# Kernel tuning notes

Measured on AMD Instinct MI355X. Metric: run time of the kernel, lower is better.

Reference implementation:

```python
import jax, jax.numpy as jnp
import numpy as np

B, C, H, W = 8, 256, 128, 128
S = C // 4          # squeezed channels (squeeze_factor=4)
HEADS = 8

def _conv(x, w, pad, groups=1):
    # NCHW conv, stride 1
    return jax.lax.conv_general_dilated(
        x, w, (1, 1), [(pad, pad), (pad, pad)],
        feature_group_count=groups,
        dimension_numbers=('NCHW', 'OIHW', 'NCHW'))

def _cln(x, w, b):
    # WithBias LayerNorm over channel dim (to_3d -> LN over c -> to_4d)
    mu = jnp.mean(x, axis=1, keepdims=True)
    var = jnp.mean((x - mu) ** 2, axis=1, keepdims=True)
    return (x - mu) * jax.lax.rsqrt(var + 1e-5) * w[None, :, None, None] + b[None, :, None, None]

def setup_inputs() -> dict:
    key = jax.random.key(0)
    ks = jax.random.split(key, 14)
    r = lambda i, shape, s=0.05: jax.random.normal(ks[i], shape, jnp.float32) * s
    return dict(
        x=r(0, (B, C, H, W), 1.0),
        y=r(1, (B, C, H, W), 1.0),
        w_cq=r(2, (S, C, 3, 3)),          # compress_q
        w_ckv=r(3, (S, C, 3, 3)),         # compress_kv
        ln_q_w=jnp.ones(S), ln_q_b=jnp.zeros(S),
        ln_kv_w=jnp.ones(S), ln_kv_b=jnp.zeros(S),
        w_kv=r(4, (2 * S, S, 1, 1)),      # kv 1x1
        w_kvdw=r(5, (2 * S, 1, 3, 3)),    # kv depthwise 3x3
        w_q=r(6, (S, S, 3, 3)),           # q 3x3
        temperature=jnp.ones((HEADS, 1, 1)),
        w_po=r(7, (S, S, 1, 1)),          # project_out 1x1
        w_expand=r(8, (C, S, 3, 3)),      # expand 3x3
        ln_out_w=jnp.ones(C), ln_out_b=jnp.zeros(C),
        w_ffn1=r(9, (C, 2 * C, 1, 1)),    # ffn conv1x1 (dim_q+dim_kv -> dim_out)
        w_ffn_dw=r(10, (C, 1, 3, 3)),     # ffn depthwise 3x3
        w_ffn2=r(11, (C, C, 1, 1)),       # ffn conv1x1
    )

def reference(x, y, w_cq, w_ckv, ln_q_w, ln_q_b, ln_kv_w, ln_kv_b,
              w_kv, w_kvdw, w_q, temperature, w_po, w_expand,
              ln_out_w, ln_out_b, w_ffn1, w_ffn_dw, w_ffn2):
    # channel compress + LayerNorm
    xq = _cln(_conv(x, w_cq, 1), ln_q_w, ln_q_b)      # [B,S,H,W]
    ykv = _cln(_conv(y, w_ckv, 1), ln_kv_w, ln_kv_b)  # [B,S,H,W]
    b, c, h, w = xq.shape
    # cross channel attention
    kv = _conv(_conv(ykv, w_kv, 0), w_kvdw, 1, groups=2 * c)
    k, v = jnp.split(kv, 2, axis=1)
    q = _conv(xq, w_q, 1)
    sh = lambda t: t.reshape(b, HEADS, c // HEADS, h * w)  # b head c (hw)
    q, k, v = sh(q), sh(k), sh(v)
    q = q / jnp.maximum(jnp.linalg.norm(q, axis=-1, keepdims=True), 1e-12)
    k = k / jnp.maximum(jnp.linalg.norm(k, axis=-1, keepdims=True), 1e-12)
    attn = jax.nn.softmax(
        jnp.einsum('bhcn,bhdn->bhcd', q, k) * temperature[None], axis=-1)
    o = jnp.einsum('bhcd,bhdn->bhcn', attn, v).reshape(b, c, h, w)
    o = _conv(o, w_po, 0)
    # expand back to full channels, norm, conv FFN
    vexp = _conv(o, w_expand, 1)                      # [B,C,H,W]
    vn = _cln(vexp, ln_out_w, ln_out_b)
    cat = jnp.concatenate([x, vn], axis=1)            # [B,2C,H,W]
    f = _conv(cat, w_ffn1, 0)
    f = jax.nn.gelu(_conv(f, w_ffn_dw, 1, groups=f.shape[1]), approximate=False)
    return _conv(f, w_ffn2, 0)
```

## Files before the change

kernel.cpp:

```cpp
#include <hip/hip_runtime.h>
#include <hip/hip_bf16.h>
#include <math.h>

#define B_ 8
#define C_ 256
#define S_ 64
#define H_ 128
#define W_ 128
#define HW_ (H_*W_)
#define P_ (B_*HW_)

typedef __attribute__((ext_vector_type(8))) short short8;
typedef __attribute__((ext_vector_type(4))) float f32x4;

__device__ __forceinline__ unsigned short f2b(float f){
    __hip_bfloat16 h = __float2bfloat16(f);
    return *reinterpret_cast<unsigned short*>(&h);
}
__device__ __forceinline__ void up8(uint4 u, float* f){
    unsigned v0=u.x,v1=u.y,v2=u.z,v3=u.w;
    f[0]=__uint_as_float(v0<<16); f[1]=__uint_as_float(v0&0xffff0000u);
    f[2]=__uint_as_float(v1<<16); f[3]=__uint_as_float(v1&0xffff0000u);
    f[4]=__uint_as_float(v2<<16); f[5]=__uint_as_float(v2&0xffff0000u);
    f[6]=__uint_as_float(v3<<16); f[7]=__uint_as_float(v3&0xffff0000u);
}
__device__ __forceinline__ uint4 pk8(const float* f){
    uint4 u;
    u.x = (unsigned)f2b(f[0]) | ((unsigned)f2b(f[1])<<16);
    u.y = (unsigned)f2b(f[2]) | ((unsigned)f2b(f[3])<<16);
    u.z = (unsigned)f2b(f[4]) | ((unsigned)f2b(f[5])<<16);
    u.w = (unsigned)f2b(f[6]) | ((unsigned)f2b(f[7])<<16);
    return u;
}
__device__ __forceinline__ void gl2lds(const unsigned short* g, unsigned short* l){
    __builtin_amdgcn_global_load_lds((const __attribute__((address_space(1))) void*)g,
                                     (__attribute__((address_space(3))) void*)l, 16, 0, 0);
}


__global__ __launch_bounds__(256) void pack_k(const float* __restrict__ inA,
                                              const float* __restrict__ inB,
                                              unsigned short* __restrict__ outA,
                                              unsigned short* __restrict__ outB)
{
    __shared__ unsigned short tl[64][72];
    const int t = threadIdx.x;
    const int p0 = blockIdx.x*64, c0 = blockIdx.y*64;
    const int sel = blockIdx.z >> 3, b = blockIdx.z & 7;
    const float* in = sel ? inB : inA;
    unsigned short* out = sel ? outB : outA;
    const float* ib = in + ((size_t)b*C_ + c0)*HW_ + p0;
    for (int i = t; i < 1024; i += 256){
        int ci = i >> 4, px = (i & 15)*4;
        float4 v = *(const float4*)(ib + (size_t)ci*HW_ + px);
        tl[px+0][ci]=f2b(v.x); tl[px+1][ci]=f2b(v.y); tl[px+2][ci]=f2b(v.z); tl[px+3][ci]=f2b(v.w);
    }
    __syncthreads();
    for (int i = t; i < 512; i += 256){
        int px = i >> 3, c8 = (i & 7)*8;
        int cc = c0 + c8;
        unsigned short* dst = out + ((size_t)b*8 + (cc>>5))*(size_t)HW_*32
                                  + (size_t)(p0+px)*32 + (cc&31);
        *(uint4*)dst = *(uint4*)&tl[px][c8];
    }
}

__device__ __forceinline__ void packw(const float* __restrict__ src, unsigned short* __restrict__ dst,
                                      int e, int CO, int CI, int KS2)
{
    int KB = CI/32;
    int tap = e / (CO*CI);
    int rem = e % (CO*CI);
    int coT = rem / (CI*16);
    int rem2 = rem % (CI*16);
    int kb = rem2 >> 9;
    int l  = (rem2 >> 3) & 63;
    int ee = rem2 & 7;
    int co = coT*16 + (l & 15);
    int ci = kb*32 + (l >> 4)*8 + ee;
    float v = (KS2==9) ? src[(size_t)(co*CI+ci)*9 + tap] : src[(size_t)co*CI + ci];
    dst[e] = f2b(v);
}

__global__ __launch_bounds__(256) void prep_k(const float* __restrict__ cq, const float* __restrict__ ckv,
                                              const float* __restrict__ q,  const float* __restrict__ kv,
                                              const float* __restrict__ f1, const float* __restrict__ f2,
                                              const float* __restrict__ dwk, const float* __restrict__ dwf,
                                              unsigned short* o_cq, unsigned short* o_ckv, unsigned short* o_q,
                                              unsigned short* o_kv, unsigned short* o_f1, unsigned short* o_f2,
                                              unsigned short* o_dwk, unsigned short* o_dwf)
{
    int i = blockIdx.x*256 + threadIdx.x;
    if      (i < 147456) packw(cq,  o_cq,  i,          64, 256, 9);
    else if (i < 294912) packw(ckv, o_ckv, i-147456,   64, 256, 9);
    else if (i < 331776) packw(q,   o_q,   i-294912,   64,  64, 9);
    else if (i < 339968) packw(kv,  o_kv,  i-331776,  128,  64, 1);
    else if (i < 471040) packw(f1,  o_f1,  i-339968,  256, 512, 1);
    else if (i < 536576) packw(f2,  o_f2,  i-471040,  256, 256, 1);
    else if (i < 537728) { int e=i-536576; o_dwk[e] = f2b(dwk[(e&127)*9 + (e>>7)]); }
    else if (i < 540032) { int e=i-537728; o_dwf[e] = f2b(dwf[(e&255)*9 + (e>>8)]); }
    else if (i < 540040) { o_dwf[i-537728] = 0; }
}

template<int C0,int C1,int COUT,int KS,int OUTM,int LNF>
__global__ __launch_bounds__(256,4) void mconv_k(
    const unsigned short* __restrict__ in0, int s0,
    const unsigned short* __restrict__ in1, int s1,
    const unsigned short* __restrict__ wp, long wpbs,
    void* __restrict__ outp, int so,
    const unsigned short* __restrict__ in0B,
    const unsigned short* __restrict__ wpB2,
    void* __restrict__ outB,
    const unsigned short* __restrict__ zbuf,
    const float* __restrict__ lnw0, const float* __restrict__ lnb0,
    const float* __restrict__ lnw1, const float* __restrict__ lnb1,
    int ny, int nz)
{
    constexpr int CINT = C0+C1;
    constexpr int KB  = CINT/32;
    constexpr int MT  = 4;
    constexpr int NT  = 2;
    constexpr int PXS = (KS==3)?66:128;
    constexpr int ASZ = (KS==3)? 4*66*32 : 8192;
    constexpr int EP  = (OUTM==1) ? 64*132*2 : 128*64;
    constexpr int SSZ = (2*ASZ > EP) ? 2*ASZ : EP;
    __shared__ alignas(16) unsigned short sbuf[SSZ];

    const int t = threadIdx.x;
    const int nper = (128*ny*nz) >> 3;
    int lin = (blockIdx.x & 7)*nper + (blockIdx.x >> 3);
    const int gy_ = lin % ny;
    int rem = lin / ny;
    const int gx_ = rem & 127;
    const int gz_ = rem >> 7;
    const int sel = gz_ >> 3;
    const int b   = gz_ & 7;
    const int cob = gy_*64;

    const unsigned short* pin0 = sel ? in0B : in0;
    const unsigned short* wpb  = (sel ? wpB2 : wp) + (size_t)b*wpbs;

    int y0=0,x0=0; size_t p0=0;
    if (KS==3){ y0=(gx_>>1)*2; x0=(gx_&1)*64; }
    else p0 = (size_t)gx_*128;

    const int l = t&63, w = t>>6;
    const int wy = w>>1, wx = w&1;
    const int lrow = l&15, lk = l>>4;

    const size_t b0base = (size_t)b*HW_*s0;
    const size_t b1base = (size_t)b*HW_*s1;

    auto issueA3 = [&](int kb, int bsel){
        const int cg = kb*32;
        unsigned short* dst = sbuf + bsel*ASZ;
        #pragma unroll
        for (int j=0;j<5;++j){
            int i = t + j*256;
            if (j<4 || i<1056){
                int slot = i&3, pr = i>>2;
                int px = pr%66, row = pr/66;
                int g = slot ^ (px&3) ^ ((px>>2)&3);
                int c = cg + g*8;
                int gy = y0+row-1, gx = x0+px-1;
                bool ok = ((unsigned)gy<(unsigned)H_) & ((unsigned)gx<(unsigned)W_);
                size_t p = (size_t)gy*W_+gx;
                const unsigned short* base = (c<C0)
                    ? pin0 + b0base + ((size_t)(c>>5)*HW_ + p)*32 + (c&31)
                    : in1  + b1base + ((size_t)((c-C0)>>5)*HW_ + p)*32 + ((c-C0)&31);
                gl2lds(ok ? base : zbuf, dst + (size_t)i*8);
            }
        }
    };
    auto issueA1 = [&](int s, int bsel){
        unsigned short* dst = sbuf + bsel*ASZ;
        #pragma unroll
        for (int h=0;h<2;++h){
            const int cg = (s*2+h)*32;
            #pragma unroll
            for (int j=0;j<2;++j){
                int i = t + j*256;
                int slot = i&3, px = i>>2;
                int g = slot ^ (px&3) ^ ((px>>2)&3);
                int c = cg + g*8;
                size_t p = p0+px;
                const unsigned short* sp = (c<C0)
                    ? pin0 + b0base + ((size_t)(c>>5)*HW_ + p)*32 + (c&31)
                    : in1  + b1base + ((size_t)((c-C0)>>5)*HW_ + p)*32 + ((c-C0)&31);
                gl2lds(sp, dst + (size_t)(h*4096 + i*8));
            }
        }
    };
    auto loadB = [&](short8* dst, int kb, int tap){
        #pragma unroll
        for (int n=0;n<NT;++n){
            int fi = (tap*(COUT/16) + (cob>>4) + wx*NT + n)*KB + kb;
            dst[n] = *(const short8*)(wpb + (size_t)fi*512 + l*8);
        }
    };

    f32x4 acc[MT][NT] = {};

    if (KS==3){
        short8 bfs[3][NT];
        issueA3(0,0);
        loadB(bfs[0],0,0); loadB(bfs[1],0,1); loadB(bfs[2],0,2);
        for (int kb=0; kb<KB; ++kb){
            __syncthreads();
            if (kb+1<KB) issueA3(kb+1,(kb+1)&1);
            unsigned short* cur = sbuf + (kb&1)*ASZ;
            #pragma unroll
            for (int tap=0;tap<9;++tap){
                const int ky=tap/3, kx=tap%3;
                short8 af[MT];
                #pragma unroll
                for (int m=0;m<MT;++m){
                    int pl = wy*64 + m*16 + lrow;
                    int r = (pl>>6)+ky, xx = (pl&63)+kx;
                    af[m] = *(const short8*)&cur[((r*PXS+xx)*4 + (lk^(xx&3)^((xx>>2)&3)))*8];
                }
                #pragma unroll
                for (int m=0;m<MT;++m)
                    #pragma unroll
                    for (int n=0;n<NT;++n)
                        acc[m][n] = __builtin_amdgcn_mfma_f32_16x16x32_bf16(af[m],bfs[tap%3][n],acc[m][n],0,0,0);
                if (tap+3 < 9)      loadB(bfs[tap%3], kb, tap+3);
                else if (kb+1<KB)   loadB(bfs[tap%3], kb+1, tap-6);
            }
        }
    } else {
        constexpr int KBS = (KB>=2) ? KB/2 : 1;
        short8 bfs[2][NT];
        issueA1(0,0);
        loadB(bfs[0],0,0); loadB(bfs[1],1,0);
        for (int s=0; s<KBS; ++s){
            __syncthreads();
            if (s+1<KBS) issueA1(s+1,(s+1)&1);
            unsigned short* cur = sbuf + (s&1)*ASZ;
            #pragma unroll
            for (int j=0;j<2;++j){
                short8 af[MT];
                #pragma unroll
                for (int m=0;m<MT;++m){
                    int pl = wy*64 + m*16 + lrow;
                    af[m] = *(const short8*)&cur[j*4096 + (pl*4 + (lk^(pl&3)^((pl>>2)&3)))*8];
                }
                #pragma unroll
                for (int m=0;m<MT;++m)
                    #pragma unroll
                    for (int n=0;n<NT;++n)
                        acc[m][n] = __builtin_amdgcn_mfma_f32_16x16x32_bf16(af[m],bfs[j][n],acc[m][n],0,0,0);
                if (s*2+j+2 < KB) loadB(bfs[j], s*2+j+2, 0);
            }
        }
    }
    __syncthreads();

    if (OUTM==1){
        float* sf = (float*)sbuf;
        #pragma unroll
        for (int m=0;m<MT;++m)
            #pragma unroll
            for (int n=0;n<NT;++n){
                int co_l = wx*32 + n*16 + lrow;
                int pl0  = wy*64 + m*16 + lk*4;
                *(f32x4*)&sf[co_l*132 + pl0] = acc[m][n];
            }
        __syncthreads();
        float* out = (float*)(sel ? outB : outp);
        for (int i=t; i<2048; i+=256){
            int co = i>>5, pxg = i&31;
            f32x4 v = *(const f32x4*)&sf[co*132 + pxg*4];
            *(f32x4*)(out + ((size_t)(b*COUT + cob + co))*HW_ + p0 + pxg*4) = v;
        }
    } else if (LNF){
        #pragma unroll
        for (int m=0;m<MT;++m)
            #pragma unroll
            for (int n=0;n<NT;++n){
                int co = wx*32 + n*16 + lrow;
                int grp = co>>3, cr = co&7;
                #pragma unroll
                for (int r=0;r<4;++r){
                    int pl = wy*64 + m*16 + lk*4 + r;
                    sbuf[pl*64 + ((grp^(pl&7))<<3) + cr] = f2b(acc[m][n][r]);
                }
            }
        __syncthreads();
        if (t < 128){
            int pl = t;
            uint4 raw[8];
            float s = 0.f, ss = 0.f;
            #pragma unroll
            for (int j=0;j<8;++j){
                raw[j] = *(const uint4*)&sbuf[pl*64 + ((j^(pl&7))<<3)];
                float f[8]; up8(raw[j], f);
                #pragma unroll
                for (int k=0;k<8;++k){ s += f[k]; ss += f[k]*f[k]; }
            }
            float mu = s*(1.f/64.f);
            float rs = rsqrtf(ss*(1.f/64.f) - mu*mu + 1e-5f);
            const float* lw = sel ? lnw1 : lnw0;
            const float* lb = sel ? lnb1 : lnb0;
            unsigned short* out = (unsigned short*)(sel ? outB : outp);
            size_t p = (size_t)(y0+(pl>>6))*W_ + x0 + (pl&63);
            #pragma unroll
            for (int j=0;j<8;++j){
                float f[8], o[8];
                up8(raw[j], f);
                #pragma unroll
                for (int k=0;k<8;++k) o[k] = (f[k]-mu)*rs*lw[j*8+k] + lb[j*8+k];
                int cc = j*8;
                unsigned short* dst = out + ((size_t)b*2 + (cc>>5))*(size_t)HW_*32 + p*32 + (cc&31);
                *(uint4*)dst = pk8(o);
            }
        }
    } else {
        unsigned short* out = (unsigned short*)(sel ? outB : outp);
        #pragma unroll
        for (int m=0;m<MT;++m)
            #pragma unroll
            for (int n=0;n<NT;++n){
                int co = wx*32 + n*16 + lrow;
                #pragma unroll
                for (int r=0;r<4;++r){
                    int pl = wy*64 + m*16 + lk*4 + r;
                    sbuf[pl*64 + co] = f2b(acc[m][n][r]);
                }
            }
        __syncthreads();
        for (int i=t; i<1024; i+=256){
            int pl = i>>3, c8 = (i&7)*8;
            size_t p = (KS==3) ? ((size_t)(y0+(pl>>6))*W_ + (size_t)(x0+(pl&63))) : (p0+pl);
            int cc = cob + c8;
            unsigned short* dst = out + (size_t)b*HW_*so + ((size_t)(cc>>5)*HW_ + p)*32 + (cc&31);
            *(uint4*)dst = *(uint4*)&sbuf[pl*64 + c8];
        }
    }
}

template<int C>
__global__ __launch_bounds__(256) void cln_k(unsigned short* __restrict__ io,
                                             const float* __restrict__ wg,
                                             const float* __restrict__ bi)
{
    constexpr int L = C/8;
    size_t idx = (size_t)blockIdx.x*256 + threadIdx.x;
    int sub = (int)(idx % L);
    size_t pix = idx / L;
    int b = (int)(pix >> 14);
    size_t p = pix & (HW_-1);
    unsigned short* rp = io + ((size_t)b*(C/32) + (sub>>2))*(size_t)HW_*32 + p*32 + (sub&3)*8;
    uint4 raw = *(const uint4*)rp;
    float f[8]; up8(raw, f);
    float s = 0.f, ss = 0.f;
    #pragma unroll
    for (int j=0;j<8;++j){ s += f[j]; ss += f[j]*f[j]; }
    #pragma unroll
    for (int m=1;m<L;m<<=1){ s += __shfl_xor(s,m); ss += __shfl_xor(ss,m); }
    float mu = s*(1.f/C);
    float rs = rsqrtf(ss*(1.f/C) - mu*mu + 1e-5f);
    float4 w0 = *(const float4*)(wg+sub*8), w1 = *(const float4*)(wg+sub*8+4);
    float4 b0 = *(const float4*)(bi+sub*8), b1 = *(const float4*)(bi+sub*8+4);
    float o[8];
    o[0]=(f[0]-mu)*rs*w0.x+b0.x; o[1]=(f[1]-mu)*rs*w0.y+b0.y;
    o[2]=(f[2]-mu)*rs*w0.z+b0.z; o[3]=(f[3]-mu)*rs*w0.w+b0.w;
    o[4]=(f[4]-mu)*rs*w1.x+b1.x; o[5]=(f[5]-mu)*rs*w1.y+b1.y;
    o[6]=(f[6]-mu)*rs*w1.z+b1.z; o[7]=(f[7]-mu)*rs*w1.w+b1.w;
    *(uint4*)rp = pk8(o);
}

template<int CH, bool GELU>
__global__ __launch_bounds__(256) void dw_k(const unsigned short* __restrict__ in,
                                            const unsigned short* __restrict__ wp,
                                            unsigned short* __restrict__ out)
{
    size_t idx = (size_t)blockIdx.x*256 + threadIdx.x;
    int c8 = (int)(idx % (CH/8));
    size_t pix = idx / (CH/8);
    int p = (int)(pix % HW_);
    int b = (int)(pix / HW_);
    int yy = p >> 7, xx = p & 127;
    const unsigned short* ib = in + ((size_t)b*(CH/32) + (c8>>2))*(size_t)HW_*32 + (c8&3)*8;
    float wf[9][8];
    #pragma unroll
    for (int tap=0; tap<9; ++tap){
        uint4 r = *(const uint4*)(wp + tap*CH + c8*8);
        up8(r, wf[tap]);
    }
    float a[8] = {0,0,0,0,0,0,0,0};
    #pragma unroll
    for (int ky=0; ky<3; ++ky){
        int gy = yy+ky-1;
        if ((unsigned)gy >= (unsigned)H_) continue;
        #pragma unroll
        for (int kx=0; kx<3; ++kx){
            int gx = xx+kx-1;
            if ((unsigned)gx >= (unsigned)W_) continue;
            uint4 r = *(const uint4*)(ib + (size_t)(gy*W_+gx)*32);
            float f[8]; up8(r, f);
            #pragma unroll
            for (int j=0;j<8;++j) a[j] += f[j]*wf[ky*3+kx][j];
        }
    }
    if (GELU){
        #pragma unroll
        for (int j=0;j<8;++j) a[j] = 0.5f*a[j]*(1.f + erff(a[j]*0.70710678118654752f));
    }
    unsigned short* ob = out + ((size_t)b*(CH/32) + (c8>>2))*(size_t)HW_*32 + (size_t)p*32 + (c8&3)*8;
    *(uint4*)ob = pk8(a);
}

__global__ __launch_bounds__(256) void attn_k(const unsigned short* __restrict__ qc,
                                              const unsigned short* __restrict__ kvd,
                                              const float* __restrict__ temp,
                                              float* __restrict__ probs)
{
    int b = blockIdx.x >> 3, h = blockIdx.x & 7;
    int t = threadIdx.x;
    const unsigned short* qb = qc  + ((size_t)b*2 + (h>>2))*(size_t)HW_*32 + (h&3)*8;
    const unsigned short* kb = kvd + ((size_t)b*4 + (h>>2))*(size_t)HW_*32 + (h&3)*8;
    float qs[8] = {}, ks[8] = {}, dt[8][8] = {{}};
    for (int p = t; p < HW_; p += 256){
        float qv[8], kv[8];
        up8(*(const uint4*)(qb + (size_t)p*32), qv);
        up8(*(const uint4*)(kb + (size_t)p*32), kv);
        #pragma unroll
        for (int i=0;i<8;++i){ qs[i]+=qv[i]*qv[i]; ks[i]+=kv[i]*kv[i]; }
        #pragma unroll
        for (int i=0;i<8;++i)
            #pragma unroll
            for (int j=0;j<8;++j) dt[i][j] += qv[i]*kv[j];
    }
    __shared__ float red[4][80];
    __shared__ float fin[80];
    int lane = t & 63, wv = t >> 6;
    #pragma unroll
    for (int i=0;i<8;++i){ float v=qs[i]; for (int m=1;m<64;m<<=1) v += __shfl_xor(v,m); if(!lane) red[wv][i]=v; }
    #pragma unroll
    for (int i=0;i<8;++i){ float v=ks[i]; for (int m=1;m<64;m<<=1) v += __shfl_xor(v,m); if(!lane) red[wv][8+i]=v; }
    #pragma unroll
    for (int i=0;i<8;++i)
        #pragma unroll
        for (int j=0;j<8;++j){ float v=dt[i][j]; for (int m=1;m<64;m<<=1) v += __shfl_xor(v,m); if(!lane) red[wv][16+i*8+j]=v; }
    __syncthreads();
    if (t < 80) fin[t] = red[0][t]+red[1][t]+red[2][t]+red[3][t];
    __syncthreads();
    if (t < 8){
        int i = t;
        float qn = fmaxf(sqrtf(fin[i]), 1e-12f);
        float tm = temp[h];
        float lg[8]; float mx = -1e30f;
        #pragma unroll
        for (int j=0;j<8;++j){
            float kn = fmaxf(sqrtf(fin[8+j]), 1e-12f);
            lg[j] = fin[16+i*8+j]/(qn*kn)*tm;
            mx = fmaxf(mx, lg[j]);
        }
        float se = 0.f;
        #pragma unroll
        for (int j=0;j<8;++j){ lg[j]=expf(lg[j]-mx); se+=lg[j]; }
        float inv = 1.f/se;
        #pragma unroll
        for (int j=0;j<8;++j) probs[(((size_t)b*8+h)*8+i)*8+j] = lg[j]*inv;
    }
}

__global__ __launch_bounds__(256) void mb_k(const float* __restrict__ probs,
                                            const float* __restrict__ wpo,
                                            float* __restrict__ Mb)
{
    int b = blockIdx.x;
    for (int o = threadIdx.x; o < 4096; o += 256){
        int co = o >> 6, d = o & 63, h = d >> 3, j = d & 7;
        float s = 0.f;
        #pragma unroll
        for (int i2=0;i2<8;++i2)
            s += wpo[co*64 + h*8 + i2] * probs[(((size_t)b*8+h)*8+i2)*8 + j];
        Mb[(size_t)b*4096 + o] = s;
    }
}

__global__ __launch_bounds__(256) void weff_k(const float* __restrict__ Mb,
                                              const float* __restrict__ wex,
                                              unsigned short* __restrict__ weff)
{
    int b = blockIdx.x / 576;
    int i = (blockIdx.x % 576)*256 + threadIdx.x;
    int tap = i / 16384;
    int rem = i % 16384;
    int coT = rem / 1024;
    int rem2 = rem % 1024;
    int kb = rem2 >> 9;
    int l  = (rem2 >> 3) & 63;
    int ee = rem2 & 7;
    int eo = coT*16 + (l & 15);
    int d  = kb*32 + (l >> 4)*8 + ee;
    const float* mb = Mb + (size_t)b*4096;
    float s = 0.f;
    #pragma unroll 8
    for (int c=0;c<64;++c)
        s += wex[(size_t)(eo*64+c)*9 + tap] * mb[c*64 + d];
    weff[(size_t)b*147456 + i] = f2b(s);
}

extern "C" void kernel_launch(void* const* d_in, const int* in_sizes, int n_in,
                              void* d_out, int out_size, void* d_ws, size_t ws_size,
                              hipStream_t stream) {
    (void)in_sizes; (void)n_in; (void)out_size; (void)ws_size;
    const float* x        = (const float*)d_in[0];
    const float* y        = (const float*)d_in[1];
    const float* w_cq     = (const float*)d_in[2];
    const float* w_ckv    = (const float*)d_in[3];
    const float* ln_q_w   = (const float*)d_in[4];
    const float* ln_q_b   = (const float*)d_in[5];
    const float* ln_kv_w  = (const float*)d_in[6];
    const float* ln_kv_b  = (const float*)d_in[7];
    const float* w_kv     = (const float*)d_in[8];
    const float* w_kvdw   = (const float*)d_in[9];
    const float* w_q      = (const float*)d_in[10];
    const float* temperature = (const float*)d_in[11];
    const float* w_po     = (const float*)d_in[12];
    const float* w_expand = (const float*)d_in[13];
    const float* ln_out_w = (const float*)d_in[14];
    const float* ln_out_b = (const float*)d_in[15];
    const float* w_ffn1   = (const float*)d_in[16];
    const float* w_ffn_dw = (const float*)d_in[17];
    const float* w_ffn2   = (const float*)d_in[18];
    float* outp = (float*)d_out;

    const size_t MB = 1u<<20;
    char* ws8 = (char*)d_ws;
    unsigned short* ykv  = (unsigned short*)(ws8 + 0);
    unsigned short* xq   = (unsigned short*)(ws8 + 16*MB);
    unsigned short* kv1  = (unsigned short*)(ws8 + 32*MB);
    unsigned short* qc   = (unsigned short*)(ws8 + 64*MB);
    unsigned short* kvd  = (unsigned short*)(ws8 + 80*MB);
    unsigned short* vexp = (unsigned short*)(ws8 + 0);
    unsigned short* f2b_ = (unsigned short*)(ws8 + 0);
    float* probs = (float*)(ws8 + 112*MB);
    float* Mb    = (float*)(ws8 + 113*MB);
    unsigned short* weff = (unsigned short*)(ws8 + 114*MB);
    unsigned short* wpB  = (unsigned short*)(ws8 + 117*MB);
    unsigned short* wp_cq  = wpB;
    unsigned short* wp_ckv = wpB + 147456;
    unsigned short* wp_q   = wpB + 294912;
    unsigned short* wp_kv  = wpB + 331776;
    unsigned short* wp_f1  = wpB + 339968;
    unsigned short* wp_f2  = wpB + 471040;
    unsigned short* wp_dwk = wpB + 536576;
    unsigned short* wp_dwf = wpB + 537728;
    unsigned short* zbuf   = wpB + 540032;
    unsigned short* xb = (unsigned short*)d_out;
    unsigned short* yb = (unsigned short*)d_out + 32*MB;
    unsigned short* f1 = yb;

    const unsigned short* NUL = (const unsigned short*)nullptr;

    prep_k<<<2111, 256, 0, stream>>>(w_cq, w_ckv, w_q, w_kv, w_ffn1, w_ffn2, w_kvdw, w_ffn_dw,
                                     wp_cq, wp_ckv, wp_q, wp_kv, wp_f1, wp_f2, wp_dwk, wp_dwf);
    pack_k<<<dim3(256,4,16), 256, 0, stream>>>(y, x, yb, xb);
    mconv_k<256,0,64,3,0,1><<<128*1*16, 256, 0, stream>>>(yb,256, NUL,0, wp_ckv,0, ykv,64,
        xb, wp_cq, xq, zbuf, ln_kv_w, ln_kv_b, ln_q_w, ln_q_b, 1, 16);
    mconv_k<64,0,128,1,0,0><<<128*2*8, 256, 0, stream>>>(ykv,64, NUL,0, wp_kv,0, kv1,128,
        ykv, wp_kv, kv1, zbuf, NULL,NULL,NULL,NULL, 2, 8);
    mconv_k<64,0,64,3,0,0><<<128*1*8, 256, 0, stream>>>(xq,64, NUL,0, wp_q,0, qc,64,
        xq, wp_q, qc, zbuf, NULL,NULL,NULL,NULL, 1, 8);
    dw_k<128,false><<<8192, 256, 0, stream>>>(kv1, wp_dwk, kvd);
    attn_k<<<64, 256, 0, stream>>>(qc, kvd, temperature, probs);
    mb_k<<<8, 256, 0, stream>>>(probs, w_po, Mb);
    weff_k<<<4608, 256, 0, stream>>>(Mb, w_expand, weff);
    mconv_k<64,0,256,3,0,0><<<128*4*8, 256, 0, stream>>>(kvd + (size_t)HW_*64,128, NUL,0, weff,147456, vexp,256,
        kvd + (size_t)HW_*64, weff, vexp, zbuf, NULL,NULL,NULL,NULL, 4, 8);
    cln_k<256><<<16384, 256, 0, stream>>>(vexp, ln_out_w, ln_out_b);
    mconv_k<256,256,256,1,0,0><<<128*4*8, 256, 0, stream>>>(xb,256, vexp,256, wp_f1,0, f1,256,
        xb, wp_f1, f1, zbuf, NULL,NULL,NULL,NULL, 4, 8);
    dw_k<256,true><<<16384, 256, 0, stream>>>(f1, wp_dwf, f2b_);
    mconv_k<256,0,256,1,1,0><<<128*4*8, 256, 0, stream>>>(f2b_,256, NUL,0, wp_f2,0, outp,0,
        f2b_, wp_f2, outp, zbuf, NULL,NULL,NULL,NULL, 4, 8);
}
```

Baseline: 519.3 us.

## Double pixel tile per block in mconv_k and widen warp N-tiles

```diff
diff --git a/kernel.cpp b/kernel.cpp
--- a/kernel.cpp
+++ b/kernel.cpp
@@ -103,7 +103,7 @@
 }
 
 template<int C0,int C1,int COUT,int KS,int OUTM,int LNF>
-__global__ __launch_bounds__(256,4) void mconv_k(
+__global__ __launch_bounds__(256,3) void mconv_k(
     const unsigned short* __restrict__ in0, int s0,
     const unsigned short* __restrict__ in1, int s1,
     const unsigned short* __restrict__ wp, long wpbs,
@@ -119,20 +119,21 @@
     constexpr int CINT = C0+C1;
     constexpr int KB  = CINT/32;
     constexpr int MT  = 4;
-    constexpr int NT  = 2;
-    constexpr int PXS = (KS==3)?66:128;
-    constexpr int ASZ = (KS==3)? 4*66*32 : 8192;
-    constexpr int EP  = (OUTM==1) ? 64*132*2 : 128*64;
+    constexpr int NT  = 4;
+    constexpr int PXS = (KS==3)?66:256;
+    constexpr int NTR = (KS==3)? 6*66*4 : 256*4;
+    constexpr int ASZ = NTR*8;
+    constexpr int EP  = (OUTM==1) ? 64*132*2 : 256*64;
     constexpr int SSZ = (2*ASZ > EP) ? 2*ASZ : EP;
     __shared__ alignas(16) unsigned short sbuf[SSZ];
 
     const int t = threadIdx.x;
-    const int nper = (128*ny*nz) >> 3;
+    const int nper = (64*ny*nz) >> 3;
     int lin = (blockIdx.x & 7)*nper + (blockIdx.x >> 3);
     const int gy_ = lin % ny;
     int rem = lin / ny;
-    const int gx_ = rem & 127;
-    const int gz_ = rem >> 7;
+    const int gx_ = rem & 63;
+    const int gz_ = rem >> 6;
     const int sel = gz_ >> 3;
     const int b   = gz_ & 7;
     const int cob = gy_*64;
@@ -141,11 +142,10 @@
     const unsigned short* wpb  = (sel ? wpB2 : wp) + (size_t)b*wpbs;
 
     int y0=0,x0=0; size_t p0=0;
-    if (KS==3){ y0=(gx_>>1)*2; x0=(gx_&1)*64; }
-    else p0 = (size_t)gx_*128;
-
-    const int l = t&63, w = t>>6;
-    const int wy = w>>1, wx = w&1;
+    if (KS==3){ y0=(gx_>>1)*4; x0=(gx_&1)*64; }
+    else p0 = (size_t)gx_*256;
+
+    const int l = t&63, wv = t>>6;
     const int lrow = l&15, lk = l>>4;
 
     const size_t b0base = (size_t)b*HW_*s0;
@@ -155,9 +155,9 @@
         const int cg = kb*32;
         unsigned short* dst = sbuf + bsel*ASZ;
         #pragma unroll
-        for (int j=0;j<5;++j){
+        for (int j=0;j<7;++j){
             int i = t + j*256;
-            if (j<4 || i<1056){
+            if (j<6 || i<1584){
                 int slot = i&3, pr = i>>2;
                 int px = pr%66, row = pr/66;
                 int g = slot ^ (px&3) ^ ((px>>2)&3);
@@ -172,29 +172,26 @@
             }
         }
     };
-    auto issueA1 = [&](int s, int bsel){
+    auto issueA1 = [&](int kb, int bsel){
+        const int cg = kb*32;
         unsigned short* dst = sbuf + bsel*ASZ;
         #pragma unroll
-        for (int h=0;h<2;++h){
-            const int cg = (s*2+h)*32;
-            #pragma unroll
-            for (int j=0;j<2;++j){
-                int i = t + j*256;
-                int slot = i&3, px = i>>2;
-                int g = slot ^ (px&3) ^ ((px>>2)&3);
-                int c = cg + g*8;
-                size_t p = p0+px;
-                const unsigned short* sp = (c<C0)
-                    ? pin0 + b0base + ((size_t)(c>>5)*HW_ + p)*32 + (c&31)
-                    : in1  + b1base + ((size_t)((c-C0)>>5)*HW_ + p)*32 + ((c-C0)&31);
-                gl2lds(sp, dst + (size_t)(h*4096 + i*8));
-            }
+        for (int j=0;j<4;++j){
+            int i = t + j*256;
+            int slot = i&3, px = i>>2;
+            int g = slot ^ (px&3) ^ ((px>>2)&3);
+            int c = cg + g*8;
+            size_t p = p0+px;
+            const unsigned short* sp = (c<C0)
+                ? pin0 + b0base + ((size_t)(c>>5)*HW_ + p)*32 + (c&31)
+                : in1  + b1base + ((size_t)((c-C0)>>5)*HW_ + p)*32 + ((c-C0)&31);
+            gl2lds(sp, dst + (size_t)i*8);
         }
     };
     auto loadB = [&](short8* dst, int kb, int tap){
         #pragma unroll
         for (int n=0;n<NT;++n){
-            int fi = (tap*(COUT/16) + (cob>>4) + wx*NT + n)*KB + kb;
+            int fi = (tap*(COUT/16) + (cob>>4) + n)*KB + kb;
             dst[n] = *(const short8*)(wpb + (size_t)fi*512 + l*8);
         }
     };
@@ -215,8 +212,8 @@
                 short8 af[MT];
                 #pragma unroll
                 for (int m=0;m<MT;++m){
-                    int pl = wy*64 + m*16 + lrow;
-                    int r = (pl>>6)+ky, xx = (pl&63)+kx;
+                    int r = wv + ky;
+                    int xx = m*16 + lrow + kx;
                     af[m] = *(const short8*)&cur[((r*PXS+xx)*4 + (lk^(xx&3)^((xx>>2)&3)))*8];
                 }
                 #pragma unroll
@@ -229,65 +226,67 @@
             }
         }
     } else {
-        constexpr int KBS = (KB>=2) ? KB/2 : 1;
         short8 bfs[2][NT];
         issueA1(0,0);
-        loadB(bfs[0],0,0); loadB(bfs[1],1,0);
-        for (int s=0; s<KBS; ++s){
+        loadB(bfs[0],0,0); if (KB>1) loadB(bfs[1],1,0);
+        for (int kb=0; kb<KB; ++kb){
             __syncthreads();
-            if (s+1<KBS) issueA1(s+1,(s+1)&1);
-            unsigned short* cur = sbuf + (s&1)*ASZ;
-            #pragma unroll
-            for (int j=0;j<2;++j){
-                short8 af[MT];
-                #pragma unroll
-                for (int m=0;m<MT;++m){
-                    int pl = wy*64 + m*16 + lrow;
-                    af[m] = *(const short8*)&cur[j*4096 + (pl*4 + (lk^(pl&3)^((pl>>2)&3)))*8];
-                }
+            if (kb+1<KB) issueA1(kb+1,(kb+1)&1);
+            unsigned short* cur = sbuf + (kb&1)*ASZ;
+            short8 af[MT];
+            #pragma unroll
+            for (int m=0;m<MT;++m){
+                int pl = wv*64 + m*16 + lrow;
+                af[m] = *(const short8*)&cur[(pl*4 + (lk^(pl&3)^((pl>>2)&3)))*8];
+            }
+            #pragma unroll
+            for (int m=0;m<MT;++m)
+                #pragma unroll
+                for (int n=0;n<NT;++n)
+                    acc[m][n] = __builtin_amdgcn_mfma_f32_16x16x32_bf16(af[m],bfs[kb&1][n],acc[m][n],0,0,0);
+            if (kb+2<KB) loadB(bfs[kb&1], kb+2, 0);
+        }
+    }
+    __syncthreads();
+
+    if (OUTM==1){
+        float* sf = (float*)sbuf;
+        float* out = (float*)(sel ? outB : outp);
+        #pragma unroll
+        for (int h=0; h<2; ++h){
+            if ((wv>>1)==h){
                 #pragma unroll
                 for (int m=0;m<MT;++m)
                     #pragma unroll
-                    for (int n=0;n<NT;++n)
-                        acc[m][n] = __builtin_amdgcn_mfma_f32_16x16x32_bf16(af[m],bfs[j][n],acc[m][n],0,0,0);
-                if (s*2+j+2 < KB) loadB(bfs[j], s*2+j+2, 0);
-            }
-        }
-    }
-    __syncthreads();
-
-    if (OUTM==1){
-        float* sf = (float*)sbuf;
+                    for (int n=0;n<NT;++n){
+                        int co = n*16 + lrow;
+                        int pll = (wv&1)*64 + m*16 + lk*4;
+                        *(f32x4*)&sf[co*132 + pll] = acc[m][n];
+                    }
+            }
+            __syncthreads();
+            for (int i=t; i<2048; i+=256){
+                int co = i>>5, pxg = i&31;
+                f32x4 v = *(const f32x4*)&sf[co*132 + pxg*4];
+                *(f32x4*)(out + ((size_t)(b*COUT + cob + co))*HW_ + p0 + h*128 + pxg*4) = v;
+            }
+            if (h==0) __syncthreads();
+        }
+    } else if (LNF){
         #pragma unroll
         for (int m=0;m<MT;++m)
             #pragma unroll
             for (int n=0;n<NT;++n){
-                int co_l = wx*32 + n*16 + lrow;
-                int pl0  = wy*64 + m*16 + lk*4;
-                *(f32x4*)&sf[co_l*132 + pl0] = acc[m][n];
-            }
-        __syncthreads();
-        float* out = (float*)(sel ? outB : outp);
-        for (int i=t; i<2048; i+=256){
-            int co = i>>5, pxg = i&31;
-            f32x4 v = *(const f32x4*)&sf[co*132 + pxg*4];
-            *(f32x4*)(out + ((size_t)(b*COUT + cob + co))*HW_ + p0 + pxg*4) = v;
-        }
-    } else if (LNF){
-        #pragma unroll
-        for (int m=0;m<MT;++m)
-            #pragma unroll
-            for (int n=0;n<NT;++n){
-                int co = wx*32 + n*16 + lrow;
+                int co = n*16 + lrow;
                 int grp = co>>3, cr = co&7;
                 #pragma unroll
                 for (int r=0;r<4;++r){
-                    int pl = wy*64 + m*16 + lk*4 + r;
+                    int pl = wv*64 + m*16 + lk*4 + r;
                     sbuf[pl*64 + ((grp^(pl&7))<<3) + cr] = f2b(acc[m][n][r]);
                 }
             }
         __syncthreads();
-        if (t < 128){
+        {
             int pl = t;
             uint4 raw[8];
             float s = 0.f, ss = 0.f;
@@ -321,15 +320,15 @@
         for (int m=0;m<MT;++m)
             #pragma unroll
             for (int n=0;n<NT;++n){
-                int co = wx*32 + n*16 + lrow;
+                int co = n*16 + lrow;
                 #pragma unroll
                 for (int r=0;r<4;++r){
-                    int pl = wy*64 + m*16 + lk*4 + r;
+                    int pl = wv*64 + m*16 + lk*4 + r;
                     sbuf[pl*64 + co] = f2b(acc[m][n][r]);
                 }
             }
         __syncthreads();
-        for (int i=t; i<1024; i+=256){
+        for (int i=t; i<2048; i+=256){
             int pl = i>>3, c8 = (i&7)*8;
             size_t p = (KS==3) ? ((size_t)(y0+(pl>>6))*W_ + (size_t)(x0+(pl&63))) : (p0+pl);
             int cc = cob + c8;
@@ -560,22 +559,22 @@
     prep_k<<<2111, 256, 0, stream>>>(w_cq, w_ckv, w_q, w_kv, w_ffn1, w_ffn2, w_kvdw, w_ffn_dw,
                                      wp_cq, wp_ckv, wp_q, wp_kv, wp_f1, wp_f2, wp_dwk, wp_dwf);
     pack_k<<<dim3(256,4,16), 256, 0, stream>>>(y, x, yb, xb);
-    mconv_k<256,0,64,3,0,1><<<128*1*16, 256, 0, stream>>>(yb,256, NUL,0, wp_ckv,0, ykv,64,
+    mconv_k<256,0,64,3,0,1><<<64*1*16, 256, 0, stream>>>(yb,256, NUL,0, wp_ckv,0, ykv,64,
         xb, wp_cq, xq, zbuf, ln_kv_w, ln_kv_b, ln_q_w, ln_q_b, 1, 16);
-    mconv_k<64,0,128,1,0,0><<<128*2*8, 256, 0, stream>>>(ykv,64, NUL,0, wp_kv,0, kv1,128,
+    mconv_k<64,0,128,1,0,0><<<64*2*8, 256, 0, stream>>>(ykv,64, NUL,0, wp_kv,0, kv1,128,
         ykv, wp_kv, kv1, zbuf, NULL,NULL,NULL,NULL, 2, 8);
-    mconv_k<64,0,64,3,0,0><<<128*1*8, 256, 0, stream>>>(xq,64, NUL,0, wp_q,0, qc,64,
+    mconv_k<64,0,64,3,0,0><<<64*1*8, 256, 0, stream>>>(xq,64, NUL,0, wp_q,0, qc,64,
         xq, wp_q, qc, zbuf, NULL,NULL,NULL,NULL, 1, 8);
     dw_k<128,false><<<8192, 256, 0, stream>>>(kv1, wp_dwk, kvd);
     attn_k<<<64, 256, 0, stream>>>(qc, kvd, temperature, probs);
     mb_k<<<8, 256, 0, stream>>>(probs, w_po, Mb);
     weff_k<<<4608, 256, 0, stream>>>(Mb, w_expand, weff);
-    mconv_k<64,0,256,3,0,0><<<128*4*8, 256, 0, stream>>>(kvd + (size_t)HW_*64,128, NUL,0, weff,147456, vexp,256,
+    mconv_k<64,0,256,3,0,0><<<64*4*8, 256, 0, stream>>>(kvd + (size_t)HW_*64,128, NUL,0, weff,147456, vexp,256,
         kvd + (size_t)HW_*64, weff, vexp, zbuf, NULL,NULL,NULL,NULL, 4, 8);
     cln_k<256><<<16384, 256, 0, stream>>>(vexp, ln_out_w, ln_out_b);
-    mconv_k<256,256,256,1,0,0><<<128*4*8, 256, 0, stream>>>(xb,256, vexp,256, wp_f1,0, f1,256,
+    mconv_k<256,256,256,1,0,0><<<64*4*8, 256, 0, stream>>>(xb,256, vexp,256, wp_f1,0, f1,256,
         xb, wp_f1, f1, zbuf, NULL,NULL,NULL,NULL, 4, 8);
     dw_k<256,true><<<16384, 256, 0, stream>>>(f1, wp_dwf, f2b_);
-    mconv_k<256,0,256,1,1,0><<<128*4*8, 256, 0, stream>>>(f2b_,256, NUL,0, wp_f2,0, outp,0,
+    mconv_k<256,0,256,1,1,0><<<64*4*8, 256, 0, stream>>>(f2b_,256, NUL,0, wp_f2,0, outp,0,
         f2b_, wp_f2, outp, zbuf, NULL,NULL,NULL,NULL, 4, 8);
 }
```

Result: slower. 573.2 us (+10.4%).
